# Optimization experiments

Hardware: AMD Instinct MI355X
Metric: run time of the kernel (lower is better)

Reference implementation:

```python
import jax, jax.numpy as jnp
import numpy as np

N_NODES = 100000


def _mean_agg(x, src, dst, n_nodes):
    # mean of src-node features over in-edges of each dst node (DGL copy_u + mean)
    summed = jax.ops.segment_sum(x[src], dst, num_segments=n_nodes)  # [N, F]
    deg = jax.ops.segment_sum(jnp.ones_like(src, dtype=x.dtype), dst, num_segments=n_nodes)
    return summed / jnp.maximum(deg, 1.0)[:, None]  # nodes w/o in-edges -> 0


def _sage_conv(x, src, dst, W_self, W_neigh, b):
    # DGL SAGEConv('mean'): fc_self(h) + fc_neigh(mean_neigh(h)) + bias
    h_neigh = _mean_agg(x, src, dst, x.shape[0])
    return x @ W_self + h_neigh @ W_neigh + b


def setup_inputs() -> dict:
    key = jax.random.key(0)
    ks = jax.random.split(key, 8)
    F_IN, F_H, E = 128, 128, 1600000
    s = 1.0 / np.sqrt(F_IN)
    return {
        "x": jax.random.normal(ks[0], (N_NODES, F_IN), dtype=jnp.float32),
        "src": jax.random.randint(ks[1], (E,), 0, N_NODES, dtype=jnp.int64),
        "dst": jax.random.randint(ks[2], (E,), 0, N_NODES, dtype=jnp.int64),
        "W1_self": jax.random.normal(ks[3], (F_IN, F_H), dtype=jnp.float32) * s,
        "W1_neigh": jax.random.normal(ks[4], (F_IN, F_H), dtype=jnp.float32) * s,
        "b1": jnp.zeros((F_H,), dtype=jnp.float32),
        "W2_self": jax.random.normal(ks[5], (F_H, F_H), dtype=jnp.float32) * s,
        "W2_neigh": jax.random.normal(ks[6], (F_H, F_H), dtype=jnp.float32) * s,
        "b2": jnp.zeros((F_H,), dtype=jnp.float32),
    }


def reference(x, src, dst, W1_self, W1_neigh, b1, W2_self, W2_neigh, b2):
    h = _sage_conv(x, src, dst, W1_self, W1_neigh, b1)
    # dropout in eval mode == identity
    h = jax.nn.relu(h)
    return _sage_conv(h, src, dst, W2_self, W2_neigh, b2)
```

## Files before the change

kernel.cpp:

```cpp
#include <hip/hip_runtime.h>

#define F 128
#define NN 100000
#define NBUK 782
#define NBLK 256
#define LD 136
#define N4 (NN * F / 4)
#define N4A (N4 / 2)
#define SORT_CAP 8192

typedef __attribute__((ext_vector_type(8))) short short8;
typedef __attribute__((ext_vector_type(4))) float f32x4;
typedef __attribute__((ext_vector_type(4))) unsigned short us4;
typedef unsigned short ushort_t;

__device__ __forceinline__ ushort_t f2b(float f) {
    union { float f; unsigned u; } x;
    x.f = f;
    unsigned r = x.u + 0x7fffu + ((x.u >> 16) & 1u);
    return (ushort_t)(r >> 16);
}
__device__ __forceinline__ float b2f(ushort_t u) {
    union { unsigned u; float f; } x;
    x.u = ((unsigned)u) << 16;
    return x.f;
}

__global__ __launch_bounds__(256) void k1_fused(
    const int* __restrict__ dst, int* __restrict__ H, int E, int chunk,
    const float* __restrict__ Wa, const float* __restrict__ Wb,
    const float* __restrict__ Wc, const float* __restrict__ Wd,
    ushort_t* __restrict__ Oa, ushort_t* __restrict__ Ob,
    ushort_t* __restrict__ Oc, ushort_t* __restrict__ Od,
    const float* __restrict__ X, ushort_t* __restrict__ Y) {
    __shared__ union {
        int h[NBUK];
        float tile[32][33];
    } u;
    const int blk = blockIdx.x;
    if (blk < NBLK) {
        for (int i = threadIdx.x; i < NBUK; i += 256) u.h[i] = 0;
        __syncthreads();
        const int s0 = blk * chunk, s1 = min(E, s0 + chunk);
        for (int i = s0 + threadIdx.x; i < s1; i += 256)
            atomicAdd(&u.h[dst[i] >> 7], 1);
        __syncthreads();
        for (int i = threadIdx.x; i < NBUK; i += 256)
            H[blk * NBUK + i] = u.h[i];
    } else if (blk < NBLK + 64) {
        const int m = (blk - NBLK) >> 4;
        const int b = (blk - NBLK) & 15;
        const float* W = (m == 0) ? Wa : (m == 1) ? Wb : (m == 2) ? Wc : Wd;
        ushort_t* WT = (m == 0) ? Oa : (m == 1) ? Ob : (m == 2) ? Oc : Od;
        const int by = (b >> 2) * 32;
        const int bx = (b & 3) * 32;
        const int tx = threadIdx.x & 31, ty = threadIdx.x >> 5;
        for (int i = 0; i < 32; i += 8)
            u.tile[ty + i][tx] = W[(by + ty + i) * F + bx + tx];
        __syncthreads();
        for (int i = 0; i < 32; i += 8)
            WT[(bx + ty + i) * F + by + tx] = f2b(u.tile[tx][ty + i]);
    } else {
        const int i = (blk - NBLK - 64) * 256 + threadIdx.x;
        if (i < N4A) {
            float4 v = ((const float4*)X)[i];
            us4 o;
            o.x = f2b(v.x); o.y = f2b(v.y); o.z = f2b(v.z); o.w = f2b(v.w);
            ((us4*)Y)[i] = o;
        }
    }
}

__global__ __launch_bounds__(256) void scan_cols(int* __restrict__ H,
                                                 int* __restrict__ Htot) {
    __shared__ int s[NBLK];
    const int k = blockIdx.x;
    const int t = threadIdx.x;
    const int v = H[t * NBUK + k];
    s[t] = v;
    __syncthreads();
    for (int d = 1; d < NBLK; d <<= 1) {
        const int u = (t >= d) ? s[t - d] : 0;
        __syncthreads();
        s[t] += u;
        __syncthreads();
    }
    H[t * NBUK + k] = s[t] - v;
    if (t == NBLK - 1) Htot[k] = s[t];
}

__global__ __launch_bounds__(1024) void k2_fused(
    const int* __restrict__ Htot, int* __restrict__ boffs, int E,
    const float* __restrict__ X, ushort_t* __restrict__ Y) {
    if (blockIdx.x == 0) {
        __shared__ int tot[1024];
        const int k = threadIdx.x;
        const int v = (k < NBUK) ? Htot[k] : 0;
        tot[k] = v;
        __syncthreads();
        for (int d = 1; d < 1024; d <<= 1) {
            const int u = (k >= d) ? tot[k - d] : 0;
            __syncthreads();
            tot[k] += u;
            __syncthreads();
        }
        if (k < NBUK) boffs[k] = tot[k] - v;
        if (k == 0) boffs[NBUK] = E;
    } else {
        const int i = N4A + (blockIdx.x - 1) * 1024 + threadIdx.x;
        if (i < N4) {
            float4 v = ((const float4*)X)[i];
            us4 o;
            o.x = f2b(v.x); o.y = f2b(v.y); o.z = f2b(v.z); o.w = f2b(v.w);
            ((us4*)Y)[i] = o;
        }
    }
}

__global__ __launch_bounds__(256) void scatter2(const int* __restrict__ src,
                                                const int* __restrict__ dst,
                                                const int* __restrict__ H,
                                                const int* __restrict__ boffs,
                                                unsigned* __restrict__ pairs,
                                                int E, int chunk) {
    __shared__ int cur[NBUK];
    const int b = blockIdx.x;
    for (int i = threadIdx.x; i < NBUK; i += 256)
        cur[i] = boffs[i] + H[b * NBUK + i];
    __syncthreads();
    const int s0 = b * chunk, s1 = min(E, s0 + chunk);
    for (int i = s0 + threadIdx.x; i < s1; i += 256) {
        const int d = dst[i];
        const int p = atomicAdd(&cur[d >> 7], 1);
        pairs[p] = ((unsigned)(d & 127) << 20) | (unsigned)src[i];
    }
}

__global__ __launch_bounds__(256) void bucket_sort(const unsigned* __restrict__ pairs,
                                                   const int* __restrict__ boffs,
                                                   int* __restrict__ offs,
                                                   int* __restrict__ csr) {
    __shared__ int cnt[128], loffs[128], lcur[128];
    __shared__ unsigned sbuf[SORT_CAP];
    const int b = blockIdx.x, t = threadIdx.x;
    const int e0 = boffs[b], e1 = boffs[b + 1];
    const int n = e1 - e0;
    const int node0 = b << 7;
    const int nnode = min(128, NN - node0);
    if (t < 128) cnt[t] = 0;
    __syncthreads();
    for (int i = e0 + t; i < e1; i += 256) atomicAdd(&cnt[pairs[i] >> 20], 1);
    __syncthreads();
    if (t < 128) loffs[t] = cnt[t];
    __syncthreads();
    for (int d = 1; d < 128; d <<= 1) {
        int u = (t >= d && t < 128) ? loffs[t - d] : 0;
        __syncthreads();
        if (t < 128) loffs[t] += u;
        __syncthreads();
    }
    if (t < 128) {
        const int ex = loffs[t] - cnt[t];
        lcur[t] = ex;
        if (t < nnode) offs[node0 + t] = e0 + ex;
    }
    if (b == NBUK - 1 && t == 0) offs[NN] = e1;
    __syncthreads();

    if (n <= SORT_CAP) {
        for (int i = e0 + t; i < e1; i += 256) {
            const unsigned v = pairs[i];
            const int p = atomicAdd(&lcur[v >> 20], 1);
            sbuf[p] = v;
        }
        __syncthreads();
        for (int i = t; i < n; i += 256) {
            const unsigned v = sbuf[i];
            const int d = v >> 20;
            const int hi = loffs[d];
            const int lo = hi - cnt[d];
            int r = lo;
            for (int j = lo; j < hi; ++j) {
                const unsigned w = sbuf[j];
                r += (w < v) || (w == v && j < i);
            }
            csr[e0 + r] = (int)(v & 0xFFFFFu);
        }
    } else {
        for (int i = e0 + t; i < e1; i += 256) {
            const unsigned v = pairs[i];
            const int p = atomicAdd(&lcur[v >> 20], 1);
            csr[e0 + p] = (int)(v & 0xFFFFFu);
        }
    }
}

template <typename TOUT>
__global__ __launch_bounds__(256, 8) void sage_layer(
    const ushort_t* __restrict__ Xg,
    const int* __restrict__ offs, const int* __restrict__ csr,
    const ushort_t* __restrict__ WTs, const ushort_t* __restrict__ WTn,
    const float* __restrict__ bias,
    TOUT* __restrict__ out, int relu) {
    __shared__ __align__(16) ushort_t sX[32 * LD];
    __shared__ __align__(16) ushort_t sH[32 * LD];
    const int t = threadIdx.x;
    const int lane = t & 63;
    const int wave = t >> 6;
    const int brow0 = blockIdx.x * 32;

    {
        const ushort_t* base = Xg + (size_t)brow0 * F;
        for (int i = t; i < 32 * 16; i += 256) {
            int row = i >> 4, ch = i & 15;
            *(short8*)&sX[row * LD + ch * 8] = *(const short8*)&base[row * F + ch * 8];
        }
    }

    {
        const int slot = lane >> 4;
        const int cl = lane & 15;
        const int c8 = cl * 8;
#pragma unroll
        for (int rr = 0; rr < 2; rr++) {
            const int rloc = wave * 8 + slot * 2 + rr;
            const int row = brow0 + rloc;
            const int e0 = offs[row], e1 = offs[row + 1];
            float acc[8];
#pragma unroll
            for (int j = 0; j < 8; j++) acc[j] = 0.f;
            int e = e0;
            for (; e + 7 < e1; e += 8) {
                const int s0 = csr[e],     s1 = csr[e + 1], s2 = csr[e + 2], s3 = csr[e + 3];
                const int s4 = csr[e + 4], s5 = csr[e + 5], s6 = csr[e + 6], s7 = csr[e + 7];
                const short8 v0 = *(const short8*)&Xg[(size_t)s0 * F + c8];
                const short8 v1 = *(const short8*)&Xg[(size_t)s1 * F + c8];
                const short8 v2 = *(const short8*)&Xg[(size_t)s2 * F + c8];
                const short8 v3 = *(const short8*)&Xg[(size_t)s3 * F + c8];
                const short8 v4 = *(const short8*)&Xg[(size_t)s4 * F + c8];
                const short8 v5 = *(const short8*)&Xg[(size_t)s5 * F + c8];
                const short8 v6 = *(const short8*)&Xg[(size_t)s6 * F + c8];
                const short8 v7 = *(const short8*)&Xg[(size_t)s7 * F + c8];
#pragma unroll
                for (int j = 0; j < 8; j++) {
                    const float t01 = b2f((ushort_t)v0[j]) + b2f((ushort_t)v1[j]);
                    const float t23 = b2f((ushort_t)v2[j]) + b2f((ushort_t)v3[j]);
                    const float t45 = b2f((ushort_t)v4[j]) + b2f((ushort_t)v5[j]);
                    const float t67 = b2f((ushort_t)v6[j]) + b2f((ushort_t)v7[j]);
                    acc[j] += (t01 + t23) + (t45 + t67);
                }
            }
            for (; e + 3 < e1; e += 4) {
                const int s0 = csr[e], s1 = csr[e + 1], s2 = csr[e + 2], s3 = csr[e + 3];
                const short8 v0 = *(const short8*)&Xg[(size_t)s0 * F + c8];
                const short8 v1 = *(const short8*)&Xg[(size_t)s1 * F + c8];
                const short8 v2 = *(const short8*)&Xg[(size_t)s2 * F + c8];
                const short8 v3 = *(const short8*)&Xg[(size_t)s3 * F + c8];
#pragma unroll
                for (int j = 0; j < 8; j++) {
                    const float t01 = b2f((ushort_t)v0[j]) + b2f((ushort_t)v1[j]);
                    const float t23 = b2f((ushort_t)v2[j]) + b2f((ushort_t)v3[j]);
                    acc[j] += t01 + t23;
                }
            }
            for (; e < e1; e++) {
                const int s0 = csr[e];
                const short8 v0 = *(const short8*)&Xg[(size_t)s0 * F + c8];
#pragma unroll
                for (int j = 0; j < 8; j++) acc[j] += b2f((ushort_t)v0[j]);
            }
            const float inv = (e1 > e0) ? (1.0f / (float)(e1 - e0)) : 0.f;
            short8 o;
#pragma unroll
            for (int j = 0; j < 8; j++) o[j] = (short)f2b(acc[j] * inv);
            *(short8*)&sH[rloc * LD + c8] = o;
        }
    }
    __syncthreads();

    const int q = lane >> 4, nl = lane & 15;
    const int colbase = wave * 32;
    f32x4 acc00 = (f32x4)0.f, acc01 = (f32x4)0.f, acc10 = (f32x4)0.f, acc11 = (f32x4)0.f;
#pragma unroll
    for (int ks = 0; ks < 4; ks++) {
        const int ko = ks * 32 + q * 8;
        const short8 aS0 = *(const short8*)&sX[nl * LD + ko];
        const short8 aS1 = *(const short8*)&sX[(16 + nl) * LD + ko];
        const short8 aN0 = *(const short8*)&sH[nl * LD + ko];
        const short8 aN1 = *(const short8*)&sH[(16 + nl) * LD + ko];
        const size_t bo0 = (size_t)(colbase + nl) * F + ko;
        const size_t bo1 = (size_t)(colbase + 16 + nl) * F + ko;
        const short8 bS0 = *(const short8*)&WTs[bo0];
        const short8 bS1 = *(const short8*)&WTs[bo1];
        const short8 bN0 = *(const short8*)&WTn[bo0];
        const short8 bN1 = *(const short8*)&WTn[bo1];
        acc00 = __builtin_amdgcn_mfma_f32_16x16x32_bf16(aS0, bS0, acc00, 0, 0, 0);
        acc00 = __builtin_amdgcn_mfma_f32_16x16x32_bf16(aN0, bN0, acc00, 0, 0, 0);
        acc01 = __builtin_amdgcn_mfma_f32_16x16x32_bf16(aS0, bS1, acc01, 0, 0, 0);
        acc01 = __builtin_amdgcn_mfma_f32_16x16x32_bf16(aN0, bN1, acc01, 0, 0, 0);
        acc10 = __builtin_amdgcn_mfma_f32_16x16x32_bf16(aS1, bS0, acc10, 0, 0, 0);
        acc10 = __builtin_amdgcn_mfma_f32_16x16x32_bf16(aN1, bN0, acc10, 0, 0, 0);
        acc11 = __builtin_amdgcn_mfma_f32_16x16x32_bf16(aS1, bS1, acc11, 0, 0, 0);
        acc11 = __builtin_amdgcn_mfma_f32_16x16x32_bf16(aN1, bN1, acc11, 0, 0, 0);
    }

    const float b0 = bias[colbase + nl];
    const float b1 = bias[colbase + 16 + nl];
    if constexpr (sizeof(TOUT) == 2) {
        __syncthreads();
#pragma unroll
        for (int r = 0; r < 4; r++) {
            const int lr0 = q * 4 + r, lr1 = 16 + q * 4 + r;
            float v00 = acc00[r] + b0, v01 = acc01[r] + b1;
            float v10 = acc10[r] + b0, v11 = acc11[r] + b1;
            if (relu) {
                v00 = fmaxf(v00, 0.f); v01 = fmaxf(v01, 0.f);
                v10 = fmaxf(v10, 0.f); v11 = fmaxf(v11, 0.f);
            }
            sX[lr0 * LD + colbase + nl] = f2b(v00);
            sX[lr0 * LD + colbase + 16 + nl] = f2b(v01);
            sX[lr1 * LD + colbase + nl] = f2b(v10);
            sX[lr1 * LD + colbase + 16 + nl] = f2b(v11);
        }
        __syncthreads();
        TOUT* base = out + (size_t)brow0 * F;
        for (int i = t; i < 32 * 16; i += 256) {
            int row = i >> 4, ch = i & 15;
            *(short8*)&base[row * F + ch * 8] = *(const short8*)&sX[row * LD + ch * 8];
        }
    } else {
#pragma unroll
        for (int r = 0; r < 4; r++) {
            const int orow0 = brow0 + q * 4 + r;
            const int orow1 = brow0 + 16 + q * 4 + r;
            float v00 = acc00[r] + b0, v01 = acc01[r] + b1;
            float v10 = acc10[r] + b0, v11 = acc11[r] + b1;
            if (relu) {
                v00 = fmaxf(v00, 0.f); v01 = fmaxf(v01, 0.f);
                v10 = fmaxf(v10, 0.f); v11 = fmaxf(v11, 0.f);
            }
            out[(size_t)orow0 * F + colbase + nl] = v00;
            out[(size_t)orow0 * F + colbase + 16 + nl] = v01;
            out[(size_t)orow1 * F + colbase + nl] = v10;
            out[(size_t)orow1 * F + colbase + 16 + nl] = v11;
        }
    }
}

extern "C" void kernel_launch(void* const* d_in, const int* in_sizes, int n_in,
                              void* d_out, int out_size, void* d_ws, size_t ws_size,
                              hipStream_t stream) {
    const float* x = (const float*)d_in[0];
    const int* src = (const int*)d_in[1];
    const int* dst = (const int*)d_in[2];
    const float* W1s = (const float*)d_in[3];
    const float* W1n = (const float*)d_in[4];
    const float* b1 = (const float*)d_in[5];
    const float* W2s = (const float*)d_in[6];
    const float* W2n = (const float*)d_in[7];
    const float* b2 = (const float*)d_in[8];
    float* out = (float*)d_out;

    const int E = in_sizes[1];
    const int N = NN;
    const int E4 = (E + 3) & ~3;
    const int chunk = (E + NBLK - 1) / NBLK;

    unsigned* pairs = (unsigned*)d_ws;
    int* csr = (int*)(pairs + E4);
    ushort_t* h1 = (ushort_t*)(csr + E4);
    ushort_t* WT1s = h1 + (size_t)N * F;
    ushort_t* WT1n = WT1s + F * F;
    ushort_t* WT2s = WT1n + F * F;
    ushort_t* WT2n = WT2s + F * F;
    int* offs = (int*)(WT2n + F * F);
    int* H = offs + (N + 1);
    int* boffs = H + NBLK * NBUK;
    int* Htot = boffs + (NBUK + 1);
    ushort_t* xb = (ushort_t*)d_out;

    const int cvtA_blocks = (N4A + 255) / 256;
    k1_fused<<<NBLK + 64 + cvtA_blocks, 256, 0, stream>>>(
        dst, H, E, chunk, W1s, W1n, W2s, W2n, WT1s, WT1n, WT2s, WT2n, x, xb);
    scan_cols<<<NBUK, NBLK, 0, stream>>>(H, Htot);
    const int cvtB_blocks = (N4 - N4A + 1023) / 1024;
    k2_fused<<<1 + cvtB_blocks, 1024, 0, stream>>>(Htot, boffs, E, x, xb);
    scatter2<<<NBLK, 256, 0, stream>>>(src, dst, H, boffs, pairs, E, chunk);
    bucket_sort<<<NBUK, 256, 0, stream>>>(pairs, boffs, offs, csr);

    sage_layer<ushort_t><<<N / 32, 256, 0, stream>>>(
        xb, offs, csr, WT1s, WT1n, b1, h1, 1);
    sage_layer<float><<<N / 32, 256, 0, stream>>>(
        h1, offs, csr, WT2s, WT2n, b2, out, 0);
}
```

Before: 340.8 us.

## Pipeline neighbor gathers through LDS with async global_load_lds staging

Replaces the register-based unrolled gather in the aggregation phase with a per-wave software pipeline. CSR indices are staged into LDS and neighbor feature rows are fetched asynchronously with global_load_lds into a DEPTH-slot ring buffer. Each wave walks its 8 rows edge-group by edge-group, with four edges in flight per group, and combines partial sums with cross-lane shuffles. A fallback path handles waves whose edge count exceeds the LDS cap. The change adds about 20KB of LDS per block, drops the occupancy hint from launch_bounds, and serializes on vmcnt waits, so occupancy may fall and latency hiding may get worse.

```diff
diff --git a/kernel.cpp b/kernel.cpp
--- a/kernel.cpp
+++ b/kernel.cpp
@@ -8,6 +8,8 @@
 #define N4 (NN * F / 4)
 #define N4A (N4 / 2)
 #define SORT_CAP 8192
+#define DEPTH 4
+#define CSRCAP 256
 
 typedef __attribute__((ext_vector_type(8))) short short8;
 typedef __attribute__((ext_vector_type(4))) float f32x4;
@@ -24,6 +26,17 @@
     union { unsigned u; float f; } x;
     x.u = ((unsigned)u) << 16;
     return x.f;
+}
+
+__device__ __forceinline__ void gload_lds16(const ushort_t* g, ushort_t* l) {
+    __builtin_amdgcn_global_load_lds(
+        (const __attribute__((address_space(1))) void*)g,
+        (__attribute__((address_space(3))) void*)l, 16, 0, 0);
+}
+__device__ __forceinline__ void gload_lds4(const int* g, int* l) {
+    __builtin_amdgcn_global_load_lds(
+        (const __attribute__((address_space(1))) void*)g,
+        (__attribute__((address_space(3))) void*)l, 4, 0, 0);
 }
 
 __global__ __launch_bounds__(256) void k1_fused(
@@ -196,7 +209,7 @@
 }
 
 template <typename TOUT>
-__global__ __launch_bounds__(256, 8) void sage_layer(
+__global__ __launch_bounds__(256) void sage_layer(
     const ushort_t* __restrict__ Xg,
     const int* __restrict__ offs, const int* __restrict__ csr,
     const ushort_t* __restrict__ WTs, const ushort_t* __restrict__ WTn,
@@ -204,9 +217,12 @@
     TOUT* __restrict__ out, int relu) {
     __shared__ __align__(16) ushort_t sX[32 * LD];
     __shared__ __align__(16) ushort_t sH[32 * LD];
+    __shared__ __align__(16) ushort_t stage[4][DEPTH * 512];
+    __shared__ int csrbuf[4][CSRCAP];
+    __shared__ int ofsbuf[4][9];
     const int t = threadIdx.x;
     const int lane = t & 63;
-    const int wave = t >> 6;
+    const int wv = t >> 6;
     const int brow0 = blockIdx.x * 32;
 
     {
@@ -218,68 +234,137 @@
     }
 
     {
-        const int slot = lane >> 4;
-        const int cl = lane & 15;
-        const int c8 = cl * 8;
-#pragma unroll
-        for (int rr = 0; rr < 2; rr++) {
-            const int rloc = wave * 8 + slot * 2 + rr;
-            const int row = brow0 + rloc;
-            const int e0 = offs[row], e1 = offs[row + 1];
-            float acc[8];
-#pragma unroll
-            for (int j = 0; j < 8; j++) acc[j] = 0.f;
-            int e = e0;
-            for (; e + 7 < e1; e += 8) {
-                const int s0 = csr[e],     s1 = csr[e + 1], s2 = csr[e + 2], s3 = csr[e + 3];
-                const int s4 = csr[e + 4], s5 = csr[e + 5], s6 = csr[e + 6], s7 = csr[e + 7];
-                const short8 v0 = *(const short8*)&Xg[(size_t)s0 * F + c8];
-                const short8 v1 = *(const short8*)&Xg[(size_t)s1 * F + c8];
-                const short8 v2 = *(const short8*)&Xg[(size_t)s2 * F + c8];
-                const short8 v3 = *(const short8*)&Xg[(size_t)s3 * F + c8];
-                const short8 v4 = *(const short8*)&Xg[(size_t)s4 * F + c8];
-                const short8 v5 = *(const short8*)&Xg[(size_t)s5 * F + c8];
-                const short8 v6 = *(const short8*)&Xg[(size_t)s6 * F + c8];
-                const short8 v7 = *(const short8*)&Xg[(size_t)s7 * F + c8];
+        const int el = lane >> 4;
+        const int ch = lane & 15;
+
+        if (lane < 9) ofsbuf[wv][lane] = offs[brow0 + wv * 8 + lane];
+        asm volatile("s_waitcnt lgkmcnt(0)" ::: "memory");
+
+        const int eb = ofsbuf[wv][0];
+        const int ee = ofsbuf[wv][8];
+        const int ncsr = ee - eb;
+
+        if (ncsr > 0 && ncsr <= CSRCAP) {
+            for (int k = 0; k < ncsr; k += 64) {
+                const int gi = min(eb + k + lane, ee - 1);
+                gload_lds4(csr + gi, &csrbuf[wv][k]);
+            }
+            asm volatile("s_waitcnt vmcnt(0)" ::: "memory");
+
+            int ir = 0;
+            int ie = eb;
+            int islot = 0;
+            auto issue_one = [&]() -> bool {
+                if (ir == 8) return false;
+                int re = ofsbuf[wv][ir + 1];
+                while (ie >= re) {
+                    ir++;
+                    if (ir == 8) return false;
+                    re = ofsbuf[wv][ir + 1];
+                }
+                const int eidx = min(ie + el, re - 1);
+                const int srcv = csrbuf[wv][eidx - eb];
+                gload_lds16(Xg + (size_t)srcv * F + ch * 8,
+                            &stage[wv][(islot & (DEPTH - 1)) * 512]);
+                islot++;
+                ie = min(ie + 4, re);
+                return true;
+            };
+
+            bool more = true;
+            bool drained = false;
+            int cslot = 0;
+#pragma unroll
+            for (int p = 0; p < DEPTH; p++)
+                if (more) more = issue_one();
+
+#pragma unroll 1
+            for (int r = 0; r < 8; r++) {
+                const int rb = ofsbuf[wv][r];
+                const int re = ofsbuf[wv][r + 1];
+                float acc[8];
+#pragma unroll
+                for (int j = 0; j < 8; j++) acc[j] = 0.f;
+#pragma unroll 1
+                for (int gb = rb; gb < re; gb += 4) {
+                    if (more) {
+                        asm volatile("s_waitcnt vmcnt(3)" ::: "memory");
+                    } else if (!drained) {
+                        asm volatile("s_waitcnt vmcnt(0)" ::: "memory");
+                        drained = true;
+                    }
+                    const short8 v =
+                        *(const short8*)&stage[wv][(cslot & (DEPTH - 1)) * 512 + lane * 8];
+                    cslot++;
+                    asm volatile("s_waitcnt lgkmcnt(0)" ::: "memory");
+                    if (more) more = issue_one();
+                    const float m = (gb + el < re) ? 1.f : 0.f;
+#pragma unroll
+                    for (int j = 0; j < 8; j++) acc[j] += m * b2f((ushort_t)v[j]);
+                }
 #pragma unroll
                 for (int j = 0; j < 8; j++) {
-                    const float t01 = b2f((ushort_t)v0[j]) + b2f((ushort_t)v1[j]);
-                    const float t23 = b2f((ushort_t)v2[j]) + b2f((ushort_t)v3[j]);
-                    const float t45 = b2f((ushort_t)v4[j]) + b2f((ushort_t)v5[j]);
-                    const float t67 = b2f((ushort_t)v6[j]) + b2f((ushort_t)v7[j]);
-                    acc[j] += (t01 + t23) + (t45 + t67);
-                }
-            }
-            for (; e + 3 < e1; e += 4) {
-                const int s0 = csr[e], s1 = csr[e + 1], s2 = csr[e + 2], s3 = csr[e + 3];
-                const short8 v0 = *(const short8*)&Xg[(size_t)s0 * F + c8];
-                const short8 v1 = *(const short8*)&Xg[(size_t)s1 * F + c8];
-                const short8 v2 = *(const short8*)&Xg[(size_t)s2 * F + c8];
-                const short8 v3 = *(const short8*)&Xg[(size_t)s3 * F + c8];
-#pragma unroll
-                for (int j = 0; j < 8; j++) {
-                    const float t01 = b2f((ushort_t)v0[j]) + b2f((ushort_t)v1[j]);
-                    const float t23 = b2f((ushort_t)v2[j]) + b2f((ushort_t)v3[j]);
-                    acc[j] += t01 + t23;
-                }
-            }
-            for (; e < e1; e++) {
-                const int s0 = csr[e];
-                const short8 v0 = *(const short8*)&Xg[(size_t)s0 * F + c8];
-#pragma unroll
-                for (int j = 0; j < 8; j++) acc[j] += b2f((ushort_t)v0[j]);
-            }
-            const float inv = (e1 > e0) ? (1.0f / (float)(e1 - e0)) : 0.f;
-            short8 o;
-#pragma unroll
-            for (int j = 0; j < 8; j++) o[j] = (short)f2b(acc[j] * inv);
-            *(short8*)&sH[rloc * LD + c8] = o;
+                    acc[j] += __shfl_xor(acc[j], 16, 64);
+                    acc[j] += __shfl_xor(acc[j], 32, 64);
+                }
+                if (lane < 16) {
+                    const int d = re - rb;
+                    const float inv = (d > 0) ? (1.0f / (float)d) : 0.f;
+                    short8 o;
+#pragma unroll
+                    for (int j = 0; j < 8; j++) o[j] = (short)f2b(acc[j] * inv);
+                    *(short8*)&sH[(wv * 8 + r) * LD + lane * 8] = o;
+                }
+            }
+        } else if (ncsr > 0) {
+            const int slot = lane >> 4;
+            const int cl = lane & 15;
+            const int c8 = cl * 8;
+            for (int rr = 0; rr < 2; rr++) {
+                const int rloc = wv * 8 + slot * 2 + rr;
+                const int row = brow0 + rloc;
+                const int e0 = offs[row], e1 = offs[row + 1];
+                float acc[8];
+#pragma unroll
+                for (int j = 0; j < 8; j++) acc[j] = 0.f;
+                int e = e0;
+                for (; e + 3 < e1; e += 4) {
+                    const int s0 = csr[e], s1 = csr[e + 1], s2 = csr[e + 2], s3 = csr[e + 3];
+                    const short8 v0 = *(const short8*)&Xg[(size_t)s0 * F + c8];
+                    const short8 v1 = *(const short8*)&Xg[(size_t)s1 * F + c8];
+                    const short8 v2 = *(const short8*)&Xg[(size_t)s2 * F + c8];
+                    const short8 v3 = *(const short8*)&Xg[(size_t)s3 * F + c8];
+#pragma unroll
+                    for (int j = 0; j < 8; j++) {
+                        const float t01 = b2f((ushort_t)v0[j]) + b2f((ushort_t)v1[j]);
+                        const float t23 = b2f((ushort_t)v2[j]) + b2f((ushort_t)v3[j]);
+                        acc[j] += t01 + t23;
+                    }
+                }
+                for (; e < e1; e++) {
+                    const int s0 = csr[e];
+                    const short8 v0 = *(const short8*)&Xg[(size_t)s0 * F + c8];
+#pragma unroll
+                    for (int j = 0; j < 8; j++) acc[j] += b2f((ushort_t)v0[j]);
+                }
+                const float inv = (e1 > e0) ? (1.0f / (float)(e1 - e0)) : 0.f;
+                short8 o;
+#pragma unroll
+                for (int j = 0; j < 8; j++) o[j] = (short)f2b(acc[j] * inv);
+                *(short8*)&sH[rloc * LD + c8] = o;
+            }
+        } else {
+            if (lane < 16) {
+                short8 z = {0, 0, 0, 0, 0, 0, 0, 0};
+                for (int r = 0; r < 8; r++)
+                    *(short8*)&sH[(wv * 8 + r) * LD + lane * 8] = z;
+            }
         }
     }
     __syncthreads();
 
     const int q = lane >> 4, nl = lane & 15;
-    const int colbase = wave * 32;
+    const int colbase = wv * 32;
     f32x4 acc00 = (f32x4)0.f, acc01 = (f32x4)0.f, acc10 = (f32x4)0.f, acc11 = (f32x4)0.f;
 #pragma unroll
     for (int ks = 0; ks < 4; ks++) {
```

Result: slower. 374.7 us (+9.9%).
